# Kernel tuning notes

Measured on AMD Instinct MI355X. Metric: run time of the kernel, lower is better.

The kernel has to match this reference:

```python
import jax, jax.numpy as jnp
import numpy as np

NUM_HEADS = 16


def setup_inputs() -> dict:
    key = jax.random.key(0)
    k1, k2, k3 = jax.random.split(key, 3)
    B, N, C = 4, 2048, 1024
    x = jax.random.normal(k1, (B, N, C), dtype=jnp.float32)
    qkv_w = jax.random.normal(k2, (3 * C, C), dtype=jnp.float32) * (C ** -0.5)
    proj_w = jax.random.normal(k3, (C, C), dtype=jnp.float32) * (C ** -0.5)
    proj_b = jnp.zeros((C,), dtype=jnp.float32)
    return {"x": x, "qkv_w": qkv_w, "proj_w": proj_w, "proj_b": proj_b, "len_t": 256}


def reference(x, qkv_w, proj_w, proj_b, len_t):
    B, N, C = x.shape
    H = NUM_HEADS
    hd = C // H
    scale = hd ** -0.5
    # qkv: [B, N, 3C] -> [3, B, H, N, hd]
    qkv = (x @ qkv_w.T).reshape(B, N, 3, H, hd).transpose(2, 0, 3, 1, 4)
    q, k, v = qkv[0], qkv[1], qkv[2]
    q_s = q[:, :, len_t:]                      # [B, H, N-len_t, hd] partial queries
    attn = jnp.einsum('bhqd,bhkd->bhqk', q_s, k) * scale
    attn = jax.nn.softmax(attn, axis=-1)       # [B, H, N-len_t, N]
    x_s = jnp.einsum('bhqk,bhkd->bhqd', attn, v)
    x_s = x_s.transpose(0, 2, 1, 3).reshape(B, N - len_t, C)
    x_t = x[:, :len_t]                         # template tokens pass through
    x_out = jnp.concatenate((x_t, x_s), axis=1)
    return x_out @ proj_w.T + proj_b
```

## Files before the change

kernel.cpp:

```cpp
#include <hip/hip_runtime.h>
#include <stdint.h>

typedef unsigned short u16;
typedef __attribute__((ext_vector_type(4))) short short4v;
typedef __attribute__((ext_vector_type(8))) short short8;
typedef __attribute__((ext_vector_type(4))) float floatx4;
typedef __attribute__((ext_vector_type(4))) unsigned short u16x4;

typedef __attribute__((address_space(1))) const void* gas_ptr;
typedef __attribute__((address_space(3))) void* las_ptr;

__device__ __forceinline__ void async16(const void* g, void* l) {
    __builtin_amdgcn_global_load_lds((gas_ptr)g, (las_ptr)l, 16, 0, 0);
}

__device__ __forceinline__ u16 f2bf(float f) {
    union { float f; unsigned int u; } v; v.f = f;
    unsigned int r = v.u + 0x7fffu + ((v.u >> 16) & 1u);
    return (u16)(r >> 16);
}

__device__ __forceinline__ int pk_bf16(float a, float b) {
    return (int)((unsigned int)f2bf(a) | ((unsigned int)f2bf(b) << 16));
}

__device__ __forceinline__ int pk2(float a, float b) {
    union { float f; unsigned int u; } ua, ub;
    ua.f = a; ub.f = b;
    return (int)__builtin_amdgcn_perm(ub.u + 0x8000u, ua.u + 0x8000u, 0x07060302u);
}

__global__ void cvt_w_kernel(const float* __restrict__ src, u16* __restrict__ dst) {
    int i = blockIdx.x * 256 + threadIdx.x;
    float4 f = reinterpret_cast<const float4*>(src)[i];
    u16x4 o;
    o.x = f2bf(f.x); o.y = f2bf(f.y); o.z = f2bf(f.z); o.w = f2bf(f.w);
    reinterpret_cast<u16x4*>(dst)[i] = o;
}

__global__ void cvt_x_kernel(const float* __restrict__ x, u16* __restrict__ xb,
                             u16* __restrict__ xout) {
    int i = blockIdx.x * 256 + threadIdx.x;
    float4 f = reinterpret_cast<const float4*>(x)[i];
    u16x4 o;
    o.x = f2bf(f.x); o.y = f2bf(f.y); o.z = f2bf(f.z); o.w = f2bf(f.w);
    reinterpret_cast<u16x4*>(xb)[i] = o;
    int m = (i * 4) >> 10;
    if ((m & 2047) < 256) reinterpret_cast<u16x4*>(xout)[i] = o;
}

template<int MODE>
__global__ void __launch_bounds__(256, 2)
gemm_nt(const u16* __restrict__ A, const u16* __restrict__ B,
        u16* __restrict__ q_out, u16* __restrict__ k_out, u16* __restrict__ vt_out,
        float* __restrict__ f_out, const float* __restrict__ bias, int K) {
    __shared__ u16 As[128 * 32];
    __shared__ u16 Bs[128 * 32];
    const int tid  = threadIdx.x;
    const int lane = tid & 63;
    const int w    = tid >> 6;
    const int row0 = blockIdx.x * 128;
    const int col0 = blockIdx.y * 128;
    const int wm   = (w >> 1) * 64;
    const int wn   = (w & 1) * 64;

    floatx4 acc[4][4] = {};

    for (int k0 = 0; k0 < K; k0 += 32) {
        __syncthreads();
#pragma unroll
        for (int i = 0; i < 2; ++i) {
            int pb = w * 128 + i * 64;
            int p  = pb + lane;
            int r  = p >> 2;
            int c  = (p & 3) ^ ((r >> 1) & 3);
            async16(A + (size_t)(row0 + r) * K + (k0 + c * 8), (char*)As + pb * 16);
            async16(B + (size_t)(col0 + r) * K + (k0 + c * 8), (char*)Bs + pb * 16);
        }
        __syncthreads();

        short8 af[4], bf_[4];
#pragma unroll
        for (int t = 0; t < 4; ++t) {
            int ar = wm + t * 16 + (lane & 15);
            int ca = (lane >> 4) ^ ((ar >> 1) & 3);
            af[t]  = *(const short8*)(As + ar * 32 + ca * 8);
            int br = wn + t * 16 + (lane & 15);
            int cb = (lane >> 4) ^ ((br >> 1) & 3);
            bf_[t] = *(const short8*)(Bs + br * 32 + cb * 8);
        }
#pragma unroll
        for (int i = 0; i < 4; ++i)
#pragma unroll
            for (int j = 0; j < 4; ++j)
                acc[i][j] = __builtin_amdgcn_mfma_f32_16x16x32_bf16(af[i], bf_[j], acc[i][j], 0, 0, 0);
    }

#pragma unroll
    for (int i = 0; i < 4; ++i) {
#pragma unroll
        for (int j = 0; j < 4; ++j) {
            int gr0 = row0 + wm + i * 16 + ((lane >> 4) << 2);
            int gc  = col0 + wn + j * 16 + (lane & 15);
            if (MODE == 0) {
                int which = gc >> 10;
                int cl = gc & 1023;
                int h = cl >> 6, d = cl & 63;
                int b = gr0 >> 11, n0 = gr0 & 2047;
                int bh = b * 16 + h;
                if (which == 2) {
                    u16x4 pk;
                    pk.x = f2bf(acc[i][j][0]); pk.y = f2bf(acc[i][j][1]);
                    pk.z = f2bf(acc[i][j][2]); pk.w = f2bf(acc[i][j][3]);
                    size_t off = (size_t)bh * 131072
                               + (((size_t)(n0 >> 5) * 4 + (d >> 4)) * 64
                                  + ((n0 >> 3) & 3) * 16 + (d & 15)) * 8 + (n0 & 4);
                    *reinterpret_cast<u16x4*>(vt_out + off) = pk;
                } else {
                    u16* dst = (which == 0) ? q_out : k_out;
                    float sc = (which == 0) ? 0.18033688f : 1.0f;
#pragma unroll
                    for (int r = 0; r < 4; ++r)
                        dst[((size_t)bh * 2048 + n0 + r) * 64 + d] = f2bf(acc[i][j][r] * sc);
                }
            } else {
                float bv = bias[gc];
#pragma unroll
                for (int r = 0; r < 4; ++r)
                    f_out[(size_t)(gr0 + r) * 1024 + gc] = acc[i][j][r] + bv;
            }
        }
    }
}

__global__ void __launch_bounds__(256, 3)
flash_attn(const u16* __restrict__ Qg, const u16* __restrict__ Kg,
           const u16* __restrict__ Vf, u16* __restrict__ xout) {
    __shared__ u16 Ks[2][64 * 64];
    const int lane = threadIdx.x & 63;
    const int w    = threadIdx.x >> 6;
    const int bh   = blockIdx.x & 63;
    const int qt   = blockIdx.x >> 6;
    const int q0   = 256 + qt * 128 + w * 32;
    const size_t kvbase = (size_t)bh * 2048 * 64;

    const int m = lane & 15;
    const int g = lane >> 4;

    short8 qf[2][2];
#pragma unroll
    for (int qs = 0; qs < 2; ++qs) {
        const u16* p = Qg + kvbase + (size_t)(q0 + qs * 16 + m) * 64 + g * 8;
        qf[qs][0] = *(const short8*)(p);
        qf[qs][1] = *(const short8*)(p + 32);
    }

    const u16* vp = Vf + (size_t)bh * 131072 + lane * 8;

    const int p0 = w * 64 + lane;
#define STAGE_K(buf, kt)                                                        \
    {                                                                           \
        _Pragma("unroll")                                                       \
        for (int i = 0; i < 2; ++i) {                                           \
            int p = i * 256 + p0;                                               \
            int r = p >> 3;                                                     \
            int c = (p & 7) ^ ((((r >> 3) & 1) << 2) | (r & 3));                \
            async16(Kg + kvbase + (size_t)((kt) * 64 + r) * 64 + c * 8,         \
                    (char*)&Ks[buf][0] + p * 16);                               \
        }                                                                       \
    }

    STAGE_K(0, 0);

    float lsum[2] = {0.f, 0.f};
    floatx4 o[2][4] = {};

    const int fm = ((m >> 2) & 1) * 4 + (m & 3);

    for (int kt = 0; kt < 32; ++kt) {
        __syncthreads();
        if (kt + 1 < 32) STAGE_K((kt + 1) & 1, kt + 1);

        const u16* kbuf = &Ks[kt & 1][0];
#pragma unroll
        for (int b32 = 0; b32 < 2; ++b32) {
            short8 vfr[4];
#pragma unroll
            for (int i = 0; i < 4; ++i)
                vfr[i] = *(const short8*)(vp + (size_t)((kt * 2 + b32) * 4 + i) * 512);

            floatx4 sT[2][2];
#pragma unroll
            for (int t = 0; t < 2; ++t) {
                int r = b32 * 32 + (m >> 2) * 8 + t * 4 + (m & 3);
                short8 k0 = *(const short8*)(kbuf + r * 64 + ((g)     ^ fm) * 8);
                short8 k1 = *(const short8*)(kbuf + r * 64 + ((4 + g) ^ fm) * 8);
#pragma unroll
                for (int qs = 0; qs < 2; ++qs) {
                    floatx4 z = {-32.f, -32.f, -32.f, -32.f};
                    z = __builtin_amdgcn_mfma_f32_16x16x32_bf16(k0, qf[qs][0], z, 0, 0, 0);
                    sT[qs][t] = __builtin_amdgcn_mfma_f32_16x16x32_bf16(k1, qf[qs][1], z, 0, 0, 0);
                }
            }

#pragma unroll
            for (int qs = 0; qs < 2; ++qs) {
                float p[8];
#pragma unroll
                for (int t = 0; t < 2; ++t)
#pragma unroll
                    for (int r = 0; r < 4; ++r) {
                        p[t * 4 + r] = __builtin_amdgcn_exp2f(sT[qs][t][r]);
                        lsum[qs] += p[t * 4 + r];
                    }
                union { int i4[4]; short8 s8; } u;
                u.i4[0] = pk2(p[0], p[1]);
                u.i4[1] = pk2(p[2], p[3]);
                u.i4[2] = pk2(p[4], p[5]);
                u.i4[3] = pk2(p[6], p[7]);
#pragma unroll
                for (int i = 0; i < 4; ++i)
                    o[qs][i] = __builtin_amdgcn_mfma_f32_16x16x32_bf16(vfr[i], u.s8, o[qs][i], 0, 0, 0);
            }
        }
    }

    const int b = bh >> 4, h = bh & 15;
#pragma unroll
    for (int qs = 0; qs < 2; ++qs) {
        float ls = lsum[qs];
        ls += __shfl_xor(ls, 16);
        ls += __shfl_xor(ls, 32);
        const float inv = 1.f / ls;

        const int n = q0 + qs * 16 + m;
        u16* dst = xout + (size_t)(b * 2048 + n) * 1024 + h * 64 + (g << 2);
#pragma unroll
        for (int i = 0; i < 4; ++i) {
            union { int i2[2]; u16x4 s4; } u;
            u.i2[0] = pk_bf16(o[qs][i][0] * inv, o[qs][i][1] * inv);
            u.i2[1] = pk_bf16(o[qs][i][2] * inv, o[qs][i][3] * inv);
            *reinterpret_cast<u16x4*>(dst + i * 16) = u.s4;
        }
    }
#undef STAGE_K
}

extern "C" void kernel_launch(void* const* d_in, const int* in_sizes, int n_in,
                              void* d_out, int out_size, void* d_ws, size_t ws_size,
                              hipStream_t stream) {
    const float* x      = (const float*)d_in[0];
    const float* qkv_w  = (const float*)d_in[1];
    const float* proj_w = (const float*)d_in[2];
    const float* proj_b = (const float*)d_in[3];

    char* ws = (char*)d_ws;
    u16* xb    = (u16*)(ws);
    u16* xout  = (u16*)(ws + ((size_t)16 << 20));
    u16* wqkv  = (u16*)(ws + ((size_t)32 << 20));
    u16* wproj = (u16*)(ws + ((size_t)38 << 20));
    u16* Qb    = (u16*)(ws + ((size_t)40 << 20));
    u16* Kb    = (u16*)(ws + ((size_t)56 << 20));
    u16* Vfb   = (u16*)(ws + ((size_t)72 << 20));

    cvt_x_kernel<<<8192, 256, 0, stream>>>(x, xb, xout);
    cvt_w_kernel<<<3072, 256, 0, stream>>>(qkv_w, wqkv);
    cvt_w_kernel<<<1024, 256, 0, stream>>>(proj_w, wproj);
    gemm_nt<0><<<dim3(64, 24), 256, 0, stream>>>(xb, wqkv, Qb, Kb, Vfb, nullptr, nullptr, 1024);
    flash_attn<<<896, 256, 0, stream>>>(Qb, Kb, Vfb, xout);
    gemm_nt<1><<<dim3(64, 8), 256, 0, stream>>>(xout, wproj, nullptr, nullptr, nullptr,
                                                (float*)d_out, proj_b, 1024);
}
```

Baseline: 258.7 us.

## Store K pre-swizzled as MFMA fragments and load directly, dropping LDS staging

The QKV GEMM epilogue now writes K in a fragment-major layout matching the MFMA operand order, the same way V was already stored. The attention kernel reads K fragments straight from global memory into registers instead of double-buffering tiles through LDS. This removes the per-tile __syncthreads and shared memory use, and occupancy is raised to 4 blocks. P is now packed to bf16 by truncation instead of rounding, which saves two adds per pack but costs a little precision. In exchange, every wave re-reads K from global/L2 with no sharing inside the block, and the scattered 2-byte K stores in the GEMM epilogue may be slower.

```diff
diff --git a/kernel.cpp b/kernel.cpp
--- a/kernel.cpp
+++ b/kernel.cpp
@@ -24,10 +24,10 @@
     return (int)((unsigned int)f2bf(a) | ((unsigned int)f2bf(b) << 16));
 }
 
-__device__ __forceinline__ int pk2(float a, float b) {
+__device__ __forceinline__ int pk2t(float a, float b) {
     union { float f; unsigned int u; } ua, ub;
     ua.f = a; ub.f = b;
-    return (int)__builtin_amdgcn_perm(ub.u + 0x8000u, ua.u + 0x8000u, 0x07060302u);
+    return (int)__builtin_amdgcn_perm(ub.u, ua.u, 0x07060302u);
 }
 
 __global__ void cvt_w_kernel(const float* __restrict__ src, u16* __restrict__ dst) {
@@ -116,12 +116,20 @@
                                + (((size_t)(n0 >> 5) * 4 + (d >> 4)) * 64
                                   + ((n0 >> 3) & 3) * 16 + (d & 15)) * 8 + (n0 & 4);
                     *reinterpret_cast<u16x4*>(vt_out + off) = pk;
+                } else if (which == 1) {
+                    int f  = (n0 >> 5) * 4 + ((n0 >> 2) & 1) * 2 + (d >> 5);
+                    int g2 = (d >> 3) & 3;
+                    int m2 = 4 * ((n0 >> 3) & 3);
+                    u16* bp = k_out + (size_t)bh * 131072
+                            + (size_t)f * 512 + (g2 * 16 + m2) * 8 + (d & 7);
+#pragma unroll
+                    for (int r = 0; r < 4; ++r)
+                        bp[r * 8] = f2bf(acc[i][j][r]);
                 } else {
-                    u16* dst = (which == 0) ? q_out : k_out;
-                    float sc = (which == 0) ? 0.18033688f : 1.0f;
+                    float sc = 0.18033688f;
 #pragma unroll
                     for (int r = 0; r < 4; ++r)
-                        dst[((size_t)bh * 2048 + n0 + r) * 64 + d] = f2bf(acc[i][j][r] * sc);
+                        q_out[((size_t)bh * 2048 + n0 + r) * 64 + d] = f2bf(acc[i][j][r] * sc);
                 }
             } else {
                 float bv = bias[gc];
@@ -133,16 +141,14 @@
     }
 }
 
-__global__ void __launch_bounds__(256, 3)
-flash_attn(const u16* __restrict__ Qg, const u16* __restrict__ Kg,
+__global__ void __launch_bounds__(256, 4)
+flash_attn(const u16* __restrict__ Qg, const u16* __restrict__ Kf,
            const u16* __restrict__ Vf, u16* __restrict__ xout) {
-    __shared__ u16 Ks[2][64 * 64];
     const int lane = threadIdx.x & 63;
     const int w    = threadIdx.x >> 6;
     const int bh   = blockIdx.x & 63;
     const int qt   = blockIdx.x >> 6;
     const int q0   = 256 + qt * 128 + w * 32;
-    const size_t kvbase = (size_t)bh * 2048 * 64;
 
     const int m = lane & 15;
     const int g = lane >> 4;
@@ -150,78 +156,57 @@
     short8 qf[2][2];
 #pragma unroll
     for (int qs = 0; qs < 2; ++qs) {
-        const u16* p = Qg + kvbase + (size_t)(q0 + qs * 16 + m) * 64 + g * 8;
+        const u16* p = Qg + ((size_t)bh * 2048 + q0 + qs * 16 + m) * 64 + g * 8;
         qf[qs][0] = *(const short8*)(p);
         qf[qs][1] = *(const short8*)(p + 32);
     }
 
+    const u16* kp = Kf + (size_t)bh * 131072 + lane * 8;
     const u16* vp = Vf + (size_t)bh * 131072 + lane * 8;
-
-    const int p0 = w * 64 + lane;
-#define STAGE_K(buf, kt)                                                        \
-    {                                                                           \
-        _Pragma("unroll")                                                       \
-        for (int i = 0; i < 2; ++i) {                                           \
-            int p = i * 256 + p0;                                               \
-            int r = p >> 3;                                                     \
-            int c = (p & 7) ^ ((((r >> 3) & 1) << 2) | (r & 3));                \
-            async16(Kg + kvbase + (size_t)((kt) * 64 + r) * 64 + c * 8,         \
-                    (char*)&Ks[buf][0] + p * 16);                               \
-        }                                                                       \
-    }
-
-    STAGE_K(0, 0);
 
     float lsum[2] = {0.f, 0.f};
     floatx4 o[2][4] = {};
 
-    const int fm = ((m >> 2) & 1) * 4 + (m & 3);
-
-    for (int kt = 0; kt < 32; ++kt) {
-        __syncthreads();
-        if (kt + 1 < 32) STAGE_K((kt + 1) & 1, kt + 1);
-
-        const u16* kbuf = &Ks[kt & 1][0];
-#pragma unroll
-        for (int b32 = 0; b32 < 2; ++b32) {
-            short8 vfr[4];
+    for (int blk = 0; blk < 64; ++blk) {
+        short8 kf[2][2];
+#pragma unroll
+        for (int t = 0; t < 2; ++t)
+#pragma unroll
+            for (int h = 0; h < 2; ++h)
+                kf[t][h] = *(const short8*)(kp + (size_t)(blk * 4 + t * 2 + h) * 512);
+        short8 vfr[4];
+#pragma unroll
+        for (int i = 0; i < 4; ++i)
+            vfr[i] = *(const short8*)(vp + (size_t)(blk * 4 + i) * 512);
+
+        floatx4 sT[2][2];
+#pragma unroll
+        for (int t = 0; t < 2; ++t)
+#pragma unroll
+            for (int qs = 0; qs < 2; ++qs) {
+                floatx4 z = {-32.f, -32.f, -32.f, -32.f};
+                z = __builtin_amdgcn_mfma_f32_16x16x32_bf16(kf[t][0], qf[qs][0], z, 0, 0, 0);
+                sT[qs][t] = __builtin_amdgcn_mfma_f32_16x16x32_bf16(kf[t][1], qf[qs][1], z, 0, 0, 0);
+            }
+
+#pragma unroll
+        for (int qs = 0; qs < 2; ++qs) {
+            float p[8];
+#pragma unroll
+            for (int t = 0; t < 2; ++t)
+#pragma unroll
+                for (int r = 0; r < 4; ++r) {
+                    p[t * 4 + r] = __builtin_amdgcn_exp2f(sT[qs][t][r]);
+                    lsum[qs] += p[t * 4 + r];
+                }
+            union { int i4[4]; short8 s8; } u;
+            u.i4[0] = pk2t(p[0], p[1]);
+            u.i4[1] = pk2t(p[2], p[3]);
+            u.i4[2] = pk2t(p[4], p[5]);
+            u.i4[3] = pk2t(p[6], p[7]);
 #pragma unroll
             for (int i = 0; i < 4; ++i)
-                vfr[i] = *(const short8*)(vp + (size_t)((kt * 2 + b32) * 4 + i) * 512);
-
-            floatx4 sT[2][2];
-#pragma unroll
-            for (int t = 0; t < 2; ++t) {
-                int r = b32 * 32 + (m >> 2) * 8 + t * 4 + (m & 3);
-                short8 k0 = *(const short8*)(kbuf + r * 64 + ((g)     ^ fm) * 8);
-                short8 k1 = *(const short8*)(kbuf + r * 64 + ((4 + g) ^ fm) * 8);
-#pragma unroll
-                for (int qs = 0; qs < 2; ++qs) {
-                    floatx4 z = {-32.f, -32.f, -32.f, -32.f};
-                    z = __builtin_amdgcn_mfma_f32_16x16x32_bf16(k0, qf[qs][0], z, 0, 0, 0);
-                    sT[qs][t] = __builtin_amdgcn_mfma_f32_16x16x32_bf16(k1, qf[qs][1], z, 0, 0, 0);
-                }
-            }
-
-#pragma unroll
-            for (int qs = 0; qs < 2; ++qs) {
-                float p[8];
-#pragma unroll
-                for (int t = 0; t < 2; ++t)
-#pragma unroll
-                    for (int r = 0; r < 4; ++r) {
-                        p[t * 4 + r] = __builtin_amdgcn_exp2f(sT[qs][t][r]);
-                        lsum[qs] += p[t * 4 + r];
-                    }
-                union { int i4[4]; short8 s8; } u;
-                u.i4[0] = pk2(p[0], p[1]);
-                u.i4[1] = pk2(p[2], p[3]);
-                u.i4[2] = pk2(p[4], p[5]);
-                u.i4[3] = pk2(p[6], p[7]);
-#pragma unroll
-                for (int i = 0; i < 4; ++i)
-                    o[qs][i] = __builtin_amdgcn_mfma_f32_16x16x32_bf16(vfr[i], u.s8, o[qs][i], 0, 0, 0);
-            }
+                o[qs][i] = __builtin_amdgcn_mfma_f32_16x16x32_bf16(vfr[i], u.s8, o[qs][i], 0, 0, 0);
         }
     }
 
@@ -243,7 +228,6 @@
             *reinterpret_cast<u16x4*>(dst + i * 16) = u.s4;
         }
     }
-#undef STAGE_K
 }
 
 extern "C" void kernel_launch(void* const* d_in, const int* in_sizes, int n_in,
@@ -260,14 +244,14 @@
     u16* wqkv  = (u16*)(ws + ((size_t)32 << 20));
     u16* wproj = (u16*)(ws + ((size_t)38 << 20));
     u16* Qb    = (u16*)(ws + ((size_t)40 << 20));
-    u16* Kb    = (u16*)(ws + ((size_t)56 << 20));
+    u16* Kfb   = (u16*)(ws + ((size_t)56 << 20));
     u16* Vfb   = (u16*)(ws + ((size_t)72 << 20));
 
     cvt_x_kernel<<<8192, 256, 0, stream>>>(x, xb, xout);
     cvt_w_kernel<<<3072, 256, 0, stream>>>(qkv_w, wqkv);
     cvt_w_kernel<<<1024, 256, 0, stream>>>(proj_w, wproj);
-    gemm_nt<0><<<dim3(64, 24), 256, 0, stream>>>(xb, wqkv, Qb, Kb, Vfb, nullptr, nullptr, 1024);
-    flash_attn<<<896, 256, 0, stream>>>(Qb, Kb, Vfb, xout);
+    gemm_nt<0><<<dim3(64, 24), 256, 0, stream>>>(xb, wqkv, Qb, Kfb, Vfb, nullptr, nullptr, 1024);
+    flash_attn<<<896, 256, 0, stream>>>(Qb, Kfb, Vfb, xout);
     gemm_nt<1><<<dim3(64, 8), 256, 0, stream>>>(xout, wproj, nullptr, nullptr, nullptr,
                                                 (float*)d_out, proj_b, 1024);
 }
```

New measurement: 260.8 us. Within noise of the previous version (+0.8%).
